# Kernel optimization log

Hardware: AMD Instinct MI355X
Metric: run time of the kernel (lower is better)

## Reference

```python
import jax, jax.numpy as jnp
import numpy as np

B = 64          # batch == number of parallel fc layers used
T = 512         # sequence length
IN_FEATS = 1024
OUT_FEATS = 1024


def setup_inputs() -> dict:
    key = jax.random.key(0)
    kx, kw, kb = jax.random.split(key, 3)
    x = jax.random.normal(kx, (B, T, IN_FEATS), dtype=jnp.float32)
    # Per-sample Linear weights, stacked: W[i] is the weight of list_fc[i]
    # (torch Linear weight layout: [out_feats, in_feats])
    bound = 1.0 / np.sqrt(IN_FEATS)
    W = jax.random.uniform(kw, (B, OUT_FEATS, IN_FEATS), dtype=jnp.float32,
                           minval=-bound, maxval=bound)
    b = jax.random.uniform(kb, (B, OUT_FEATS), dtype=jnp.float32,
                           minval=-bound, maxval=bound)
    return {"x": x, "W": W, "b": b}


def reference(x, W, b):
    # Equivalent to: cat([list_fc[i](x[i:i+1]) for i in range(B)], dim=0)
    # i.e. a grouped GEMM with group size 1: out[i] = x[i] @ W[i].T + b[i]
    out = jnp.einsum('bti,boi->bto', x, W)  # [B, T, OUT]
    return out + b[:, None, :]
```

## Files before the change

### kernel.cpp

```cpp
#include <hip/hip_runtime.h>
#include <hip/hip_bf16.h>

#define BATCH 64
#define MDIM 512
#define NDIM 1024
#define KDIM 1024

#define BM 256
#define BN 256
#define BK 32
#define NT (KDIM / BK)

typedef __attribute__((ext_vector_type(4))) float f32x4;
typedef __attribute__((ext_vector_type(8))) short bf16x8;
typedef __attribute__((ext_vector_type(4))) unsigned int u32x4;

__device__ __forceinline__ unsigned int cvt2(float lo, float hi) {
    __hip_bfloat162 h = __float22bfloat162_rn(float2{lo, hi});
    return *(unsigned int*)&h;
}

__global__ __launch_bounds__(512, 2)
void grouped_fc_kernel(const float* __restrict__ X,
                       const float* __restrict__ W,
                       const float* __restrict__ Bias,
                       float* __restrict__ Out) {
    const int swz  = (blockIdx.x & 7) * 64 + (blockIdx.x >> 3);
    const int bidx = swz >> 3;
    const int tile = swz & 7;
    const int tm = tile & 1;
    const int tn = tile >> 1;

    const int tid  = threadIdx.x;
    const int lane = tid & 63;
    const int wid  = tid >> 6;
    const int wm   = wid & 1;
    const int wn   = wid >> 1;

    __shared__ unsigned short ldsA[2][BM][BK];
    __shared__ unsigned short ldsB[2][BN][BK];

    const float* srcA = X + ((size_t)bidx * MDIM + (size_t)tm * BM) * KDIM;
    const float* srcB = W + ((size_t)bidx * NDIM + (size_t)tn * BN) * KDIM;

    int s_row[2], s_c[2], s_sw[2];
#pragma unroll
    for (int g = 0; g < 2; ++g) {
        int f = tid + g * 512;
        s_row[g] = f >> 2;
        s_c[g]   = (f & 3) * 8;
        s_sw[g]  = ((f & 3) ^ ((s_row[g] >> 1) & 3)) * 8;
    }

    f32x4 va[2][2], vb[2][2];

    auto load_tiles = [&](int kt) {
#pragma unroll
        for (int g = 0; g < 2; ++g) {
            const float* pa = srcA + (size_t)s_row[g] * KDIM + kt * BK + s_c[g];
            va[g][0] = *(const f32x4*)(pa);
            va[g][1] = *(const f32x4*)(pa + 4);
            const float* pb = srcB + (size_t)s_row[g] * KDIM + kt * BK + s_c[g];
            vb[g][0] = *(const f32x4*)(pb);
            vb[g][1] = *(const f32x4*)(pb + 4);
        }
    };

    auto store_tiles = [&](int buf) {
#pragma unroll
        for (int g = 0; g < 2; ++g) {
            u32x4 wa, wb;
            wa[0] = cvt2(va[g][0][0], va[g][0][1]);
            wa[1] = cvt2(va[g][0][2], va[g][0][3]);
            wa[2] = cvt2(va[g][1][0], va[g][1][1]);
            wa[3] = cvt2(va[g][1][2], va[g][1][3]);
            wb[0] = cvt2(vb[g][0][0], vb[g][0][1]);
            wb[1] = cvt2(vb[g][0][2], vb[g][0][3]);
            wb[2] = cvt2(vb[g][1][0], vb[g][1][1]);
            wb[3] = cvt2(vb[g][1][2], vb[g][1][3]);
            *(u32x4*)&ldsA[buf][s_row[g]][s_sw[g]] = wa;
            *(u32x4*)&ldsB[buf][s_row[g]][s_sw[g]] = wb;
        }
    };

    const int frow = lane & 15;
    const int rsl  = ((lane >> 4) ^ ((frow >> 1) & 3)) * 8;

    f32x4 acc[8][4];
#pragma unroll
    for (int mi = 0; mi < 8; ++mi)
#pragma unroll
        for (int ni = 0; ni < 4; ++ni)
            acc[mi][ni] = (f32x4){0.f, 0.f, 0.f, 0.f};

    load_tiles(0);
    store_tiles(0);
    load_tiles(1);

#pragma unroll 2
    for (int kt = 0; kt < NT; ++kt) {
        const int cur = kt & 1;
        asm volatile("s_waitcnt lgkmcnt(0)" ::: "memory");
        __builtin_amdgcn_sched_barrier(0);
        __syncthreads();

        if (kt + 1 < NT) store_tiles(cur ^ 1);
        if (kt + 2 < NT) load_tiles(kt + 2);

        bf16x8 af[8], bfr[4];
#pragma unroll
        for (int mi = 0; mi < 8; ++mi)
            af[mi] = *(const bf16x8*)&ldsA[cur][wm * 128 + mi * 16 + frow][rsl];
#pragma unroll
        for (int ni = 0; ni < 4; ++ni)
            bfr[ni] = *(const bf16x8*)&ldsB[cur][wn * 64 + ni * 16 + frow][rsl];

#pragma unroll
        for (int mi = 0; mi < 8; ++mi)
#pragma unroll
            for (int ni = 0; ni < 4; ++ni)
                acc[mi][ni] = __builtin_amdgcn_mfma_f32_16x16x32_bf16(
                    af[mi], bfr[ni], acc[mi][ni], 0, 0, 0);
    }

#pragma unroll
    for (int ni = 0; ni < 4; ++ni) {
        const int gc = tn * BN + wn * 64 + ni * 16 + frow;
        const float bv = Bias[bidx * NDIM + gc];
#pragma unroll
        for (int mi = 0; mi < 8; ++mi) {
            const int gr0 = tm * BM + wm * 128 + mi * 16 + (lane >> 4) * 4;
            float* po = Out + ((size_t)bidx * MDIM + gr0) * NDIM + gc;
#pragma unroll
            for (int r = 0; r < 4; ++r)
                po[(size_t)r * NDIM] = acc[mi][ni][r] + bv;
        }
    }
}

extern "C" void kernel_launch(void* const* d_in, const int* in_sizes, int n_in,
                              void* d_out, int out_size, void* d_ws, size_t ws_size,
                              hipStream_t stream) {
    const float* X  = (const float*)d_in[0];
    const float* W  = (const float*)d_in[1];
    const float* Bs = (const float*)d_in[2];
    float* Out = (float*)d_out;

    grouped_fc_kernel<<<dim3(512), dim3(512), 0, stream>>>(X, W, Bs, Out);
}
```

Measured before the change: 156.4 us.

## Split K-loop into ping-pong MFMA phases with barriers and setprio

Restructures the main loop into two phases per K-tile, each issuing half the B-fragment MFMAs between explicit s_barriers, with s_setprio raised around the MFMA blocks. This is a ping-pong style schedule in which the global load for the next tile is issued before the first phase and the LDS write for it happens between phases. Prefetch depth drops from two tiles ahead to one, which reduces register pressure. The thread-to-tile mapping changes so each thread loads 16 contiguous floats per row, and the LDS swizzle changes to match. The intent is better overlap of memory and matrix work across the two waves per SIMD. The cost is extra barriers per iteration and less latency hiding for global loads.

```diff
diff --git a/kernel.cpp b/kernel.cpp
--- a/kernel.cpp
+++ b/kernel.cpp
@@ -9,7 +9,7 @@
 #define BM 256
 #define BN 256
 #define BK 32
-#define NT (KDIM / BK)
+#define NKT (KDIM / BK)
 
 typedef __attribute__((ext_vector_type(4))) float f32x4;
 typedef __attribute__((ext_vector_type(8))) short bf16x8;
@@ -19,6 +19,16 @@
     __hip_bfloat162 h = __float22bfloat162_rn(float2{lo, hi});
     return *(unsigned int*)&h;
 }
+
+#define PHASE_PRE  do { __builtin_amdgcn_sched_barrier(0); \
+    __builtin_amdgcn_s_barrier(); \
+    asm volatile("s_waitcnt lgkmcnt(0)" ::: "memory"); \
+    __builtin_amdgcn_sched_barrier(0); \
+    __builtin_amdgcn_s_setprio(1); } while (0)
+#define PHASE_POST do { __builtin_amdgcn_s_setprio(0); \
+    __builtin_amdgcn_sched_barrier(0); \
+    __builtin_amdgcn_s_barrier(); \
+    __builtin_amdgcn_sched_barrier(0); } while (0)
 
 __global__ __launch_bounds__(512, 2)
 void grouped_fc_kernel(const float* __restrict__ X,
@@ -43,48 +53,48 @@
     const float* srcA = X + ((size_t)bidx * MDIM + (size_t)tm * BM) * KDIM;
     const float* srcB = W + ((size_t)bidx * NDIM + (size_t)tn * BN) * KDIM;
 
-    int s_row[2], s_c[2], s_sw[2];
+    const int s_r  = tid >> 1;
+    const int s_cf = (tid & 1) * 16;
+    const int sw0  = (((tid & 1) * 2)     ^ (s_r & 3)) * 8;
+    const int sw1  = (((tid & 1) * 2 + 1) ^ (s_r & 3)) * 8;
+
+    const int frow = lane & 15;
+    const int khi  = lane >> 4;
+    const int rsl  = (khi ^ (frow & 3)) * 8;
+
+    f32x4 sa[4], sb[4];
+
+    auto LOADT = [&](int kt) {
+        const float* pa = srcA + (size_t)s_r * KDIM + kt * BK + s_cf;
+        const float* pb = srcB + (size_t)s_r * KDIM + kt * BK + s_cf;
 #pragma unroll
-    for (int g = 0; g < 2; ++g) {
-        int f = tid + g * 512;
-        s_row[g] = f >> 2;
-        s_c[g]   = (f & 3) * 8;
-        s_sw[g]  = ((f & 3) ^ ((s_row[g] >> 1) & 3)) * 8;
-    }
-
-    f32x4 va[2][2], vb[2][2];
-
-    auto load_tiles = [&](int kt) {
+        for (int v = 0; v < 4; ++v) sa[v] = *(const f32x4*)(pa + v * 4);
 #pragma unroll
-        for (int g = 0; g < 2; ++g) {
-            const float* pa = srcA + (size_t)s_row[g] * KDIM + kt * BK + s_c[g];
-            va[g][0] = *(const f32x4*)(pa);
-            va[g][1] = *(const f32x4*)(pa + 4);
-            const float* pb = srcB + (size_t)s_row[g] * KDIM + kt * BK + s_c[g];
-            vb[g][0] = *(const f32x4*)(pb);
-            vb[g][1] = *(const f32x4*)(pb + 4);
-        }
+        for (int v = 0; v < 4; ++v) sb[v] = *(const f32x4*)(pb + v * 4);
     };
 
-    auto store_tiles = [&](int buf) {
-#pragma unroll
-        for (int g = 0; g < 2; ++g) {
-            u32x4 wa, wb;
-            wa[0] = cvt2(va[g][0][0], va[g][0][1]);
-            wa[1] = cvt2(va[g][0][2], va[g][0][3]);
-            wa[2] = cvt2(va[g][1][0], va[g][1][1]);
-            wa[3] = cvt2(va[g][1][2], va[g][1][3]);
-            wb[0] = cvt2(vb[g][0][0], vb[g][0][1]);
-            wb[1] = cvt2(vb[g][0][2], vb[g][0][3]);
-            wb[2] = cvt2(vb[g][1][0], vb[g][1][1]);
-            wb[3] = cvt2(vb[g][1][2], vb[g][1][3]);
-            *(u32x4*)&ldsA[buf][s_row[g]][s_sw[g]] = wa;
-            *(u32x4*)&ldsB[buf][s_row[g]][s_sw[g]] = wb;
-        }
+    auto WRITET = [&](int buf) {
+        u32x4 wa0, wa1, wb0, wb1;
+        wa0[0] = cvt2(sa[0][0], sa[0][1]); wa0[1] = cvt2(sa[0][2], sa[0][3]);
+        wa0[2] = cvt2(sa[1][0], sa[1][1]); wa0[3] = cvt2(sa[1][2], sa[1][3]);
+        wa1[0] = cvt2(sa[2][0], sa[2][1]); wa1[1] = cvt2(sa[2][2], sa[2][3]);
+        wa1[2] = cvt2(sa[3][0], sa[3][1]); wa1[3] = cvt2(sa[3][2], sa[3][3]);
+        wb0[0] = cvt2(sb[0][0], sb[0][1]); wb0[1] = cvt2(sb[0][2], sb[0][3]);
+        wb0[2] = cvt2(sb[1][0], sb[1][1]); wb0[3] = cvt2(sb[1][2], sb[1][3]);
+        wb1[0] = cvt2(sb[2][0], sb[2][1]); wb1[1] = cvt2(sb[2][2], sb[2][3]);
+        wb1[2] = cvt2(sb[3][0], sb[3][1]); wb1[3] = cvt2(sb[3][2], sb[3][3]);
+        *(u32x4*)&ldsA[buf][s_r][sw0] = wa0;
+        *(u32x4*)&ldsA[buf][s_r][sw1] = wa1;
+        *(u32x4*)&ldsB[buf][s_r][sw0] = wb0;
+        *(u32x4*)&ldsB[buf][s_r][sw1] = wb1;
     };
 
-    const int frow = lane & 15;
-    const int rsl  = ((lane >> 4) ^ ((frow >> 1) & 3)) * 8;
+    auto rdA = [&](int buf, int mi) {
+        return *(const bf16x8*)&ldsA[buf][wm * 128 + mi * 16 + frow][rsl];
+    };
+    auto rdB = [&](int buf, int ni) {
+        return *(const bf16x8*)&ldsB[buf][wn * 64 + ni * 16 + frow][rsl];
+    };
 
     f32x4 acc[8][4];
 #pragma unroll
@@ -93,34 +103,41 @@
         for (int ni = 0; ni < 4; ++ni)
             acc[mi][ni] = (f32x4){0.f, 0.f, 0.f, 0.f};
 
-    load_tiles(0);
-    store_tiles(0);
-    load_tiles(1);
+    LOADT(0);
+    WRITET(0);
+    asm volatile("s_waitcnt lgkmcnt(0)" ::: "memory");
+    __builtin_amdgcn_s_barrier();
+    __builtin_amdgcn_sched_barrier(0);
 
-#pragma unroll 2
-    for (int kt = 0; kt < NT; ++kt) {
+#pragma unroll 1
+    for (int kt = 0; kt < NKT; ++kt) {
         const int cur = kt & 1;
-        asm volatile("s_waitcnt lgkmcnt(0)" ::: "memory");
-        __builtin_amdgcn_sched_barrier(0);
-        __syncthreads();
-
-        if (kt + 1 < NT) store_tiles(cur ^ 1);
-        if (kt + 2 < NT) load_tiles(kt + 2);
-
-        bf16x8 af[8], bfr[4];
-#pragma unroll
-        for (int mi = 0; mi < 8; ++mi)
-            af[mi] = *(const bf16x8*)&ldsA[cur][wm * 128 + mi * 16 + frow][rsl];
-#pragma unroll
-        for (int ni = 0; ni < 4; ++ni)
-            bfr[ni] = *(const bf16x8*)&ldsB[cur][wn * 64 + ni * 16 + frow][rsl];
+        const bool more = (kt + 1 < NKT);
+        bf16x8 af[8], b01[2], b23[2];
 
 #pragma unroll
-        for (int mi = 0; mi < 8; ++mi)
+        for (int mi = 0; mi < 8; ++mi) af[mi] = rdA(cur, mi);
+        b01[0] = rdB(cur, 0);
+        b01[1] = rdB(cur, 1);
+        if (more) LOADT(kt + 1);
+        PHASE_PRE;
 #pragma unroll
-            for (int ni = 0; ni < 4; ++ni)
-                acc[mi][ni] = __builtin_amdgcn_mfma_f32_16x16x32_bf16(
-                    af[mi], bfr[ni], acc[mi][ni], 0, 0, 0);
+        for (int mi = 0; mi < 8; ++mi) {
+            acc[mi][0] = __builtin_amdgcn_mfma_f32_16x16x32_bf16(af[mi], b01[0], acc[mi][0], 0, 0, 0);
+            acc[mi][1] = __builtin_amdgcn_mfma_f32_16x16x32_bf16(af[mi], b01[1], acc[mi][1], 0, 0, 0);
+        }
+        PHASE_POST;
+
+        b23[0] = rdB(cur, 2);
+        b23[1] = rdB(cur, 3);
+        if (more) WRITET(cur ^ 1);
+        PHASE_PRE;
+#pragma unroll
+        for (int mi = 0; mi < 8; ++mi) {
+            acc[mi][2] = __builtin_amdgcn_mfma_f32_16x16x32_bf16(af[mi], b23[0], acc[mi][2], 0, 0, 0);
+            acc[mi][3] = __builtin_amdgcn_mfma_f32_16x16x32_bf16(af[mi], b23[1], acc[mi][3], 0, 0, 0);
+        }
+        PHASE_POST;
     }
 
 #pragma unroll
```

Result: slower. 189.6 us (+21.3%).

## Deepen global-load pipeline to three stages with split convert/write

Applied to the files above, without the earlier changes.

Separates the fp32-to-bf16 conversion from the LDS write so that global loads are issued three K-tiles ahead, conversions one tile ahead, and LDS writes for the next buffer right after the barrier. The goal is to hide more global-memory latency behind the MFMA loop. The barrier becomes a raw s_barrier fenced by sched_barriers instead of __syncthreads. This adds registers for converted staging data, which could hurt occupancy under launch_bounds(512,2), and the less conservative barrier could allow unwanted reordering.

```diff
diff --git a/kernel.cpp b/kernel.cpp
--- a/kernel.cpp
+++ b/kernel.cpp
@@ -9,7 +9,7 @@
 #define BM 256
 #define BN 256
 #define BK 32
-#define NT (KDIM / BK)
+#define NKT (KDIM / BK)
 
 typedef __attribute__((ext_vector_type(4))) float f32x4;
 typedef __attribute__((ext_vector_type(8))) short bf16x8;
@@ -19,6 +19,12 @@
     __hip_bfloat162 h = __float22bfloat162_rn(float2{lo, hi});
     return *(unsigned int*)&h;
 }
+
+#define RELEASE_BARRIER do { \
+    asm volatile("s_waitcnt lgkmcnt(0)" ::: "memory"); \
+    __builtin_amdgcn_sched_barrier(0); \
+    __builtin_amdgcn_s_barrier(); \
+    __builtin_amdgcn_sched_barrier(0); } while (0)
 
 __global__ __launch_bounds__(512, 2)
 void grouped_fc_kernel(const float* __restrict__ X,
@@ -52,34 +58,40 @@
         s_sw[g]  = ((f & 3) ^ ((s_row[g] >> 1) & 3)) * 8;
     }
 
-    f32x4 va[2][2], vb[2][2];
+    f32x4 fa[2][2], fb[2][2];
+    u32x4 ca[2], cb[2];
 
-    auto load_tiles = [&](int kt) {
+    auto LOADT = [&](int kt) {
 #pragma unroll
         for (int g = 0; g < 2; ++g) {
             const float* pa = srcA + (size_t)s_row[g] * KDIM + kt * BK + s_c[g];
-            va[g][0] = *(const f32x4*)(pa);
-            va[g][1] = *(const f32x4*)(pa + 4);
+            fa[g][0] = *(const f32x4*)(pa);
+            fa[g][1] = *(const f32x4*)(pa + 4);
             const float* pb = srcB + (size_t)s_row[g] * KDIM + kt * BK + s_c[g];
-            vb[g][0] = *(const f32x4*)(pb);
-            vb[g][1] = *(const f32x4*)(pb + 4);
+            fb[g][0] = *(const f32x4*)(pb);
+            fb[g][1] = *(const f32x4*)(pb + 4);
         }
     };
 
-    auto store_tiles = [&](int buf) {
+    auto CVTT = [&]() {
 #pragma unroll
         for (int g = 0; g < 2; ++g) {
-            u32x4 wa, wb;
-            wa[0] = cvt2(va[g][0][0], va[g][0][1]);
-            wa[1] = cvt2(va[g][0][2], va[g][0][3]);
-            wa[2] = cvt2(va[g][1][0], va[g][1][1]);
-            wa[3] = cvt2(va[g][1][2], va[g][1][3]);
-            wb[0] = cvt2(vb[g][0][0], vb[g][0][1]);
-            wb[1] = cvt2(vb[g][0][2], vb[g][0][3]);
-            wb[2] = cvt2(vb[g][1][0], vb[g][1][1]);
-            wb[3] = cvt2(vb[g][1][2], vb[g][1][3]);
-            *(u32x4*)&ldsA[buf][s_row[g]][s_sw[g]] = wa;
-            *(u32x4*)&ldsB[buf][s_row[g]][s_sw[g]] = wb;
+            ca[g][0] = cvt2(fa[g][0][0], fa[g][0][1]);
+            ca[g][1] = cvt2(fa[g][0][2], fa[g][0][3]);
+            ca[g][2] = cvt2(fa[g][1][0], fa[g][1][1]);
+            ca[g][3] = cvt2(fa[g][1][2], fa[g][1][3]);
+            cb[g][0] = cvt2(fb[g][0][0], fb[g][0][1]);
+            cb[g][1] = cvt2(fb[g][0][2], fb[g][0][3]);
+            cb[g][2] = cvt2(fb[g][1][0], fb[g][1][1]);
+            cb[g][3] = cvt2(fb[g][1][2], fb[g][1][3]);
+        }
+    };
+
+    auto WRITET = [&](int buf) {
+#pragma unroll
+        for (int g = 0; g < 2; ++g) {
+            *(u32x4*)&ldsA[buf][s_row[g]][s_sw[g]] = ca[g];
+            *(u32x4*)&ldsB[buf][s_row[g]][s_sw[g]] = cb[g];
         }
     };
 
@@ -93,19 +105,18 @@
         for (int ni = 0; ni < 4; ++ni)
             acc[mi][ni] = (f32x4){0.f, 0.f, 0.f, 0.f};
 
-    load_tiles(0);
-    store_tiles(0);
-    load_tiles(1);
+    LOADT(0); CVTT(); WRITET(0);
+    LOADT(1); CVTT();
+    LOADT(2);
 
 #pragma unroll 2
-    for (int kt = 0; kt < NT; ++kt) {
+    for (int kt = 0; kt < NKT; ++kt) {
         const int cur = kt & 1;
-        asm volatile("s_waitcnt lgkmcnt(0)" ::: "memory");
-        __builtin_amdgcn_sched_barrier(0);
-        __syncthreads();
+        RELEASE_BARRIER;
 
-        if (kt + 1 < NT) store_tiles(cur ^ 1);
-        if (kt + 2 < NT) load_tiles(kt + 2);
+        if (kt + 1 < NKT) WRITET(cur ^ 1);
+        if (kt + 2 < NKT) CVTT();
+        if (kt + 3 < NKT) LOADT(kt + 3);
 
         bf16x8 af[8], bfr[4];
 #pragma unroll
```

Result: faster. 151.5 us (-3.1%).

## Stage fp32 tiles directly into LDS and convert to bf16 on fragment reads

Applied to the files above, without the earlier changes.

Replaces the register-staged path (global load, convert to bf16, store to LDS) with direct global-to-LDS loads of raw fp32 tiles, using an XOR swizzle on the 16-byte chunks. Fragments are converted to bf16 when they are read from LDS, and MFMA issue is wrapped in raised wave priority. This aims to free VGPRs and VALU work from the staging path and let loads overlap compute without a register round trip. In exchange, LDS use doubles to about 128KB per block, which likely allows only one block per CU instead of two. LDS read bandwidth also doubles, and each wave repeats the conversion for every fragment it reads.

```diff
diff --git a/kernel.cpp b/kernel.cpp
--- a/kernel.cpp
+++ b/kernel.cpp
@@ -9,7 +9,7 @@
 #define BM 256
 #define BN 256
 #define BK 32
-#define NT (KDIM / BK)
+#define NKT (KDIM / BK)
 
 typedef __attribute__((ext_vector_type(4))) float f32x4;
 typedef __attribute__((ext_vector_type(8))) short bf16x8;
@@ -19,6 +19,8 @@
     __hip_bfloat162 h = __float22bfloat162_rn(float2{lo, hi});
     return *(unsigned int*)&h;
 }
+
+#define MFMA16(a, b, c) __builtin_amdgcn_mfma_f32_16x16x32_bf16((a), (b), (c), 0, 0, 0)
 
 __global__ __launch_bounds__(512, 2)
 void grouped_fc_kernel(const float* __restrict__ X,
@@ -37,54 +39,49 @@
     const int wm   = wid & 1;
     const int wn   = wid >> 1;
 
-    __shared__ unsigned short ldsA[2][BM][BK];
-    __shared__ unsigned short ldsB[2][BN][BK];
+    __shared__ float ldsA[2][BM][BK];
+    __shared__ float ldsB[2][BN][BK];
 
     const float* srcA = X + ((size_t)bidx * MDIM + (size_t)tm * BM) * KDIM;
     const float* srcB = W + ((size_t)bidx * NDIM + (size_t)tn * BN) * KDIM;
 
-    int s_row[2], s_c[2], s_sw[2];
+    const int lrow = lane >> 3;
+    const int lgr  = (lane & 7) ^ lrow;
+    const size_t lsrc = (size_t)lrow * KDIM + lgr * 4;
+
+    auto STAGE = [&](int buf, int kt) {
 #pragma unroll
-    for (int g = 0; g < 2; ++g) {
-        int f = tid + g * 512;
-        s_row[g] = f >> 2;
-        s_c[g]   = (f & 3) * 8;
-        s_sw[g]  = ((f & 3) ^ ((s_row[g] >> 1) & 3)) * 8;
-    }
-
-    f32x4 va[2][2], vb[2][2];
-
-    auto load_tiles = [&](int kt) {
+        for (int j = 0; j < 4; ++j) {
+            const int c = wid * 4 + j;
+            const float* ga = srcA + (size_t)c * 8 * KDIM + kt * BK + lsrc;
+            __builtin_amdgcn_global_load_lds(
+                (const __attribute__((address_space(1))) void*)ga,
+                (__attribute__((address_space(3))) void*)&ldsA[buf][c * 8][0],
+                16, 0, 0);
+        }
 #pragma unroll
-        for (int g = 0; g < 2; ++g) {
-            const float* pa = srcA + (size_t)s_row[g] * KDIM + kt * BK + s_c[g];
-            va[g][0] = *(const f32x4*)(pa);
-            va[g][1] = *(const f32x4*)(pa + 4);
-            const float* pb = srcB + (size_t)s_row[g] * KDIM + kt * BK + s_c[g];
-            vb[g][0] = *(const f32x4*)(pb);
-            vb[g][1] = *(const f32x4*)(pb + 4);
-        }
-    };
-
-    auto store_tiles = [&](int buf) {
-#pragma unroll
-        for (int g = 0; g < 2; ++g) {
-            u32x4 wa, wb;
-            wa[0] = cvt2(va[g][0][0], va[g][0][1]);
-            wa[1] = cvt2(va[g][0][2], va[g][0][3]);
-            wa[2] = cvt2(va[g][1][0], va[g][1][1]);
-            wa[3] = cvt2(va[g][1][2], va[g][1][3]);
-            wb[0] = cvt2(vb[g][0][0], vb[g][0][1]);
-            wb[1] = cvt2(vb[g][0][2], vb[g][0][3]);
-            wb[2] = cvt2(vb[g][1][0], vb[g][1][1]);
-            wb[3] = cvt2(vb[g][1][2], vb[g][1][3]);
-            *(u32x4*)&ldsA[buf][s_row[g]][s_sw[g]] = wa;
-            *(u32x4*)&ldsB[buf][s_row[g]][s_sw[g]] = wb;
+        for (int j = 0; j < 4; ++j) {
+            const int c = wid * 4 + j;
+            const float* gb = srcB + (size_t)c * 8 * KDIM + kt * BK + lsrc;
+            __builtin_amdgcn_global_load_lds(
+                (const __attribute__((address_space(1))) void*)gb,
+                (__attribute__((address_space(3))) void*)&ldsB[buf][c * 8][0],
+                16, 0, 0);
         }
     };
 
     const int frow = lane & 15;
-    const int rsl  = ((lane >> 4) ^ ((frow >> 1) & 3)) * 8;
+    const int khi  = lane >> 4;
+    const int s0   = (((khi * 2) ^ (frow & 7))) * 4;
+
+    auto RDFRAG = [&](const float* rowp) -> bf16x8 {
+        f32x4 lo = *(const f32x4*)(rowp + s0);
+        f32x4 hi = *(const f32x4*)(rowp + (s0 ^ 4));
+        u32x4 u;
+        u[0] = cvt2(lo[0], lo[1]); u[1] = cvt2(lo[2], lo[3]);
+        u[2] = cvt2(hi[0], hi[1]); u[3] = cvt2(hi[2], hi[3]);
+        return __builtin_bit_cast(bf16x8, u);
+    };
 
     f32x4 acc[8][4];
 #pragma unroll
@@ -93,34 +90,39 @@
         for (int ni = 0; ni < 4; ++ni)
             acc[mi][ni] = (f32x4){0.f, 0.f, 0.f, 0.f};
 
-    load_tiles(0);
-    store_tiles(0);
-    load_tiles(1);
+    STAGE(0, 0);
+    asm volatile("s_waitcnt vmcnt(0)" ::: "memory");
+    __builtin_amdgcn_sched_barrier(0);
+    __builtin_amdgcn_s_barrier();
+    __builtin_amdgcn_sched_barrier(0);
 
-#pragma unroll 2
-    for (int kt = 0; kt < NT; ++kt) {
-        const int cur = kt & 1;
-        asm volatile("s_waitcnt lgkmcnt(0)" ::: "memory");
-        __builtin_amdgcn_sched_barrier(0);
-        __syncthreads();
+#pragma unroll 1
+    for (int kt = 0; kt < NKT; ++kt) {
+        const int rd = kt & 1;
+        const bool m1 = (kt + 1 < NKT);
 
-        if (kt + 1 < NT) store_tiles(cur ^ 1);
-        if (kt + 2 < NT) load_tiles(kt + 2);
+        if (m1) STAGE(rd ^ 1, kt + 1);
 
         bf16x8 af[8], bfr[4];
 #pragma unroll
         for (int mi = 0; mi < 8; ++mi)
-            af[mi] = *(const bf16x8*)&ldsA[cur][wm * 128 + mi * 16 + frow][rsl];
+            af[mi] = RDFRAG(&ldsA[rd][wm * 128 + mi * 16 + frow][0]);
 #pragma unroll
         for (int ni = 0; ni < 4; ++ni)
-            bfr[ni] = *(const bf16x8*)&ldsB[cur][wn * 64 + ni * 16 + frow][rsl];
+            bfr[ni] = RDFRAG(&ldsB[rd][wn * 64 + ni * 16 + frow][0]);
 
+        __builtin_amdgcn_s_setprio(1);
 #pragma unroll
         for (int mi = 0; mi < 8; ++mi)
 #pragma unroll
             for (int ni = 0; ni < 4; ++ni)
-                acc[mi][ni] = __builtin_amdgcn_mfma_f32_16x16x32_bf16(
-                    af[mi], bfr[ni], acc[mi][ni], 0, 0, 0);
+                acc[mi][ni] = MFMA16(af[mi], bfr[ni], acc[mi][ni]);
+        __builtin_amdgcn_s_setprio(0);
+
+        asm volatile("s_waitcnt vmcnt(0)" ::: "memory");
+        __builtin_amdgcn_sched_barrier(0);
+        __builtin_amdgcn_s_barrier();
+        __builtin_amdgcn_sched_barrier(0);
     }
 
 #pragma unroll
@@ -129,7 +131,7 @@
         const float bv = Bias[bidx * NDIM + gc];
 #pragma unroll
         for (int mi = 0; mi < 8; ++mi) {
-            const int gr0 = tm * BM + wm * 128 + mi * 16 + (lane >> 4) * 4;
+            const int gr0 = tm * BM + wm * 128 + mi * 16 + khi * 4;
             float* po = Out + ((size_t)bidx * MDIM + gr0) * NDIM + gc;
 #pragma unroll
             for (int r = 0; r < 4; ++r)
```

Measured after the change: 190.9 us. 1.22x slower.
